# Performance work log

Hardware: AMD Instinct MI355X
Metric: run time of the kernel (lower is better)

The kernel has to match this reference:

```python
import jax, jax.numpy as jnp
import numpy as np


def setup_inputs() -> dict:
    key = jax.random.key(0)
    vel = jax.random.normal(key, (10000, 1000, 3), dtype=jnp.float32)
    return {"vel": vel, "vacf_window": 100}


def reference(vel, vacf_window):
    # vel: [T, N, 3]; output: [vacf_window]
    T = vel.shape[0]
    flat = vel.reshape(T, -1)  # [T, N*3]
    # lag 0: mean(vel * vel)
    terms = [jnp.mean(flat * flat)]
    # lags 1..vacf_window-1: mean over (T - t) * N * 3 elements
    for t in range(1, vacf_window):
        terms.append(jnp.mean(flat[t:] * flat[:-t]))
    return jnp.stack(terms)
```

## Files before the change

kernel.cpp:

```cpp
#include <hip/hip_runtime.h>


#define T_DIM 10000
#define C_DIM 3000
#define W 100
#define MA 256
#define NA 16
#define SROWS 384
#define NBB 40
#define KS 47
#define KW 64
#define NPART 8

typedef __attribute__((ext_vector_type(8))) short short8;
typedef __attribute__((ext_vector_type(4))) short short4v;
typedef __attribute__((ext_vector_type(4))) float float4v;

__device__ __forceinline__ short f2bf(float f) {
    unsigned u = __float_as_uint(f);
    u += 0x7fffu + ((u >> 16) & 1u);
    return (short)(u >> 16);
}

__global__ __launch_bounds__(256, 3)
void vacf_fused(const float* __restrict__ X, float* __restrict__ partial) {
    const int tid  = threadIdx.x;
    const int lane = tid & 63;
    const int wv   = tid >> 6;
    const int ksix = blockIdx.x % KS;
    const int bb   = blockIdx.x / KS;
    const int i0   = bb * MA;
    const int c0   = ksix * KW;

    __shared__ __align__(16) char lds[SROWS * 128];
    __shared__ float bins[W];
    if (tid < W) bins[tid] = 0.f;

    const int rr = tid >> 4;
    const int cl = (tid & 15) * 4;
    const int sw = ((((cl >> 3) ^ (rr & 7)) << 4) | ((cl & 7) << 1));

    const bool fast = (i0 + SROWS <= T_DIM) && (c0 + KW <= C_DIM);
    if (fast) {
        #pragma unroll
        for (int b = 0; b < 3; ++b) {
            float4v v[8];
            #pragma unroll
            for (int m = 0; m < 8; ++m) {
                const int row = b * 128 + m * 16 + rr;
                v[m] = *(const float4v*)(X + (size_t)(i0 + row) * C_DIM + c0 + cl);
            }
            #pragma unroll
            for (int m = 0; m < 8; ++m) {
                const int row = b * 128 + m * 16 + rr;
                short4v o;
                o[0] = f2bf(v[m][0]); o[1] = f2bf(v[m][1]);
                o[2] = f2bf(v[m][2]); o[3] = f2bf(v[m][3]);
                *(short4v*)&lds[row * 128 + sw] = o;
            }
        }
    } else {
        #pragma unroll
        for (int b = 0; b < 3; ++b) {
            #pragma unroll
            for (int m = 0; m < 8; ++m) {
                const int row = b * 128 + m * 16 + rr;
                const int gr  = i0 + row;
                float4v v = {0.f, 0.f, 0.f, 0.f};
                if (gr < T_DIM && c0 + cl + 4 <= C_DIM)
                    v = *(const float4v*)(X + (size_t)gr * C_DIM + c0 + cl);
                short4v o;
                o[0] = f2bf(v[0]); o[1] = f2bf(v[1]);
                o[2] = f2bf(v[2]); o[3] = f2bf(v[3]);
                *(short4v*)&lds[row * 128 + sw] = o;
            }
        }
    }
    __syncthreads();

    const int n    = lane & 15;
    const int quad = lane >> 4;
    const int d0   = 2 * wv;

    float4v acc0 = {0.f, 0.f, 0.f, 0.f};
    float4v acc1 = {0.f, 0.f, 0.f, 0.f};

    #pragma unroll
    for (int kk = 0; kk < 2; ++kk) {
        const char* lb = lds + n * 128 + (((((kk << 2) | quad)) ^ (n & 7)) << 4);
        short8 fbp = *(const short8*)(lb + d0 * 2048);
        #pragma unroll
        for (int a = 0; a < NA; ++a) {
            const short8 fav = *(const short8*)(lb + a * 2048);
            const short8 fbn = *(const short8*)(lb + (d0 + a + 1) * 2048);
            acc0 = __builtin_amdgcn_mfma_f32_16x16x32_bf16(fav, fbp, acc0, 0, 0, 0);
            acc1 = __builtin_amdgcn_mfma_f32_16x16x32_bf16(fav, fbn, acc1, 0, 0, 0);
            fbp = fbn;
        }
    }

    #pragma unroll
    for (int p = 0; p < 4; ++p) {
        const int m  = quad * 4 + p;
        const int t0 = 16 * d0 + n - m;
        if (t0 >= 0 && t0 < W) atomicAdd(&bins[t0], acc0[p]);
        const int t1 = t0 + 16;
        if (t1 >= 0 && t1 < W) atomicAdd(&bins[t1], acc1[p]);
    }
    __syncthreads();
    if (tid < W) atomicAdd(&partial[(blockIdx.x & 7) * W + tid], bins[tid]);
}

__global__ void vacf_scale(const float* __restrict__ partial, float* __restrict__ out) {
    int t = threadIdx.x;
    if (t < W) {
        float s = 0.f;
        #pragma unroll
        for (int b = 0; b < NPART; ++b) s += partial[b * W + t];
        out[t] = s / ((float)(T_DIM - t) * (float)C_DIM);
    }
}

extern "C" void kernel_launch(void* const* d_in, const int* in_sizes, int n_in,
                              void* d_out, int out_size, void* d_ws, size_t ws_size,
                              hipStream_t stream) {
    const float* X = (const float*)d_in[0];
    float* out = (float*)d_out;
    float* ws  = (float*)d_ws;

    hipMemsetAsync(ws, 0, NPART * W * sizeof(float), stream);
    vacf_fused<<<NBB * KS, 256, 0, stream>>>(X, ws);
    vacf_scale<<<1, 128, 0, stream>>>(ws, out);
}
```

Baseline: 186.7 us.

## Halve column tile width and map column strips to XCDs for L2 reuse

Each block now covers 32 columns instead of 64, which halves the LDS staging buffer and doubles the grid. Block indices are remapped so that all blocks sharing a column strip run on the same XCD, letting the 1.5x overlapping row reads hit in that XCD's L2. The atomic partial buffer is widened from 8 to 32 slots to reduce global atomic contention. In exchange, each row read is a shorter 128-byte segment and there are more blocks, each doing fewer MFMAs, so per-block fixed overhead grows.

```diff
diff --git a/kernel.cpp b/kernel.cpp
--- a/kernel.cpp
+++ b/kernel.cpp
@@ -8,9 +8,10 @@
 #define NA 16
 #define SROWS 384
 #define NBB 40
-#define KS 47
-#define KW 64
-#define NPART 8
+#define KS 96
+#define KW 32
+#define SPX 12
+#define NPART 32
 
 typedef __attribute__((ext_vector_type(8))) short short8;
 typedef __attribute__((ext_vector_type(4))) short short4v;
@@ -27,53 +28,46 @@
     const int tid  = threadIdx.x;
     const int lane = tid & 63;
     const int wv   = tid >> 6;
-    const int ksix = blockIdx.x % KS;
-    const int bb   = blockIdx.x / KS;
+    const int xcd  = blockIdx.x & 7;
+    const int u    = blockIdx.x >> 3;
+    const int ksix = xcd + 8 * (u / NBB);
+    const int bb   = u % NBB;
     const int i0   = bb * MA;
     const int c0   = ksix * KW;
 
-    __shared__ __align__(16) char lds[SROWS * 128];
+    __shared__ __align__(16) char lds[SROWS * 64];
     __shared__ float bins[W];
     if (tid < W) bins[tid] = 0.f;
 
-    const int rr = tid >> 4;
-    const int cl = (tid & 15) * 4;
-    const int sw = ((((cl >> 3) ^ (rr & 7)) << 4) | ((cl & 7) << 1));
+    const int rr = tid >> 3;
+    const int cl = (tid & 7) * 4;
+    const int sw = ((((cl >> 3) ^ ((rr >> 1) & 3)) << 4) | ((cl & 7) << 1));
 
     const bool fast = (i0 + SROWS <= T_DIM) && (c0 + KW <= C_DIM);
     if (fast) {
+        float4v v[12];
         #pragma unroll
-        for (int b = 0; b < 3; ++b) {
-            float4v v[8];
-            #pragma unroll
-            for (int m = 0; m < 8; ++m) {
-                const int row = b * 128 + m * 16 + rr;
-                v[m] = *(const float4v*)(X + (size_t)(i0 + row) * C_DIM + c0 + cl);
-            }
-            #pragma unroll
-            for (int m = 0; m < 8; ++m) {
-                const int row = b * 128 + m * 16 + rr;
-                short4v o;
-                o[0] = f2bf(v[m][0]); o[1] = f2bf(v[m][1]);
-                o[2] = f2bf(v[m][2]); o[3] = f2bf(v[m][3]);
-                *(short4v*)&lds[row * 128 + sw] = o;
-            }
+        for (int m = 0; m < 12; ++m)
+            v[m] = *(const float4v*)(X + (size_t)(i0 + m * 32 + rr) * C_DIM + c0 + cl);
+        #pragma unroll
+        for (int m = 0; m < 12; ++m) {
+            short4v o;
+            o[0] = f2bf(v[m][0]); o[1] = f2bf(v[m][1]);
+            o[2] = f2bf(v[m][2]); o[3] = f2bf(v[m][3]);
+            *(short4v*)&lds[(m * 32 + rr) * 64 + sw] = o;
         }
     } else {
         #pragma unroll
-        for (int b = 0; b < 3; ++b) {
-            #pragma unroll
-            for (int m = 0; m < 8; ++m) {
-                const int row = b * 128 + m * 16 + rr;
-                const int gr  = i0 + row;
-                float4v v = {0.f, 0.f, 0.f, 0.f};
-                if (gr < T_DIM && c0 + cl + 4 <= C_DIM)
-                    v = *(const float4v*)(X + (size_t)gr * C_DIM + c0 + cl);
-                short4v o;
-                o[0] = f2bf(v[0]); o[1] = f2bf(v[1]);
-                o[2] = f2bf(v[2]); o[3] = f2bf(v[3]);
-                *(short4v*)&lds[row * 128 + sw] = o;
-            }
+        for (int m = 0; m < 12; ++m) {
+            const int row = m * 32 + rr;
+            const int gr  = i0 + row;
+            float4v v = {0.f, 0.f, 0.f, 0.f};
+            if (gr < T_DIM && c0 + cl + 4 <= C_DIM)
+                v = *(const float4v*)(X + (size_t)gr * C_DIM + c0 + cl);
+            short4v o;
+            o[0] = f2bf(v[0]); o[1] = f2bf(v[1]);
+            o[2] = f2bf(v[2]); o[3] = f2bf(v[3]);
+            *(short4v*)&lds[row * 64 + sw] = o;
         }
     }
     __syncthreads();
@@ -85,18 +79,15 @@
     float4v acc0 = {0.f, 0.f, 0.f, 0.f};
     float4v acc1 = {0.f, 0.f, 0.f, 0.f};
 
+    const char* lb = lds + n * 64 + ((quad ^ ((n >> 1) & 3)) << 4);
+    short8 fbp = *(const short8*)(lb + d0 * 1024);
     #pragma unroll
-    for (int kk = 0; kk < 2; ++kk) {
-        const char* lb = lds + n * 128 + (((((kk << 2) | quad)) ^ (n & 7)) << 4);
-        short8 fbp = *(const short8*)(lb + d0 * 2048);
-        #pragma unroll
-        for (int a = 0; a < NA; ++a) {
-            const short8 fav = *(const short8*)(lb + a * 2048);
-            const short8 fbn = *(const short8*)(lb + (d0 + a + 1) * 2048);
-            acc0 = __builtin_amdgcn_mfma_f32_16x16x32_bf16(fav, fbp, acc0, 0, 0, 0);
-            acc1 = __builtin_amdgcn_mfma_f32_16x16x32_bf16(fav, fbn, acc1, 0, 0, 0);
-            fbp = fbn;
-        }
+    for (int a = 0; a < NA; ++a) {
+        const short8 fav = *(const short8*)(lb + a * 1024);
+        const short8 fbn = *(const short8*)(lb + (d0 + a + 1) * 1024);
+        acc0 = __builtin_amdgcn_mfma_f32_16x16x32_bf16(fav, fbp, acc0, 0, 0, 0);
+        acc1 = __builtin_amdgcn_mfma_f32_16x16x32_bf16(fav, fbn, acc1, 0, 0, 0);
+        fbp = fbn;
     }
 
     #pragma unroll
@@ -108,7 +99,7 @@
         if (t1 >= 0 && t1 < W) atomicAdd(&bins[t1], acc1[p]);
     }
     __syncthreads();
-    if (tid < W) atomicAdd(&partial[(blockIdx.x & 7) * W + tid], bins[tid]);
+    if (tid < W) atomicAdd(&partial[(blockIdx.x & (NPART - 1)) * W + tid], bins[tid]);
 }
 
 __global__ void vacf_scale(const float* __restrict__ partial, float* __restrict__ out) {
@@ -129,6 +120,6 @@
     float* ws  = (float*)d_ws;
 
     hipMemsetAsync(ws, 0, NPART * W * sizeof(float), stream);
-    vacf_fused<<<NBB * KS, 256, 0, stream>>>(X, ws);
+    vacf_fused<<<KS * NBB, 256, 0, stream>>>(X, ws);
     vacf_scale<<<1, 128, 0, stream>>>(ws, out);
 }
```

New measurement: 188.4 us. Within noise of the previous version (+0.9%).
